# Kernel optimization log

Hardware: AMD Instinct MI355X
Metric: run time of the kernel (lower is better)

Reference implementation:

```python
import jax, jax.numpy as jnp
import numpy as np

SCALE = 1.0

def setup_inputs() -> dict:
    key = jax.random.key(0)
    k1, k2 = jax.random.split(key)
    template = jax.random.normal(k1, (4, 8192, 3), dtype=jnp.float32)
    source = jax.random.normal(k2, (4, 8192, 3), dtype=jnp.float32)
    return {"template": template, "source": source}

def _chamfer(p0, p1):
    # p0: [B,N,3], p1: [B,M,3]
    # squared pairwise distances: [B,N,M]
    sq0 = jnp.sum(p0 * p0, axis=-1)  # [B,N]
    sq1 = jnp.sum(p1 * p1, axis=-1)  # [B,M]
    cross = jnp.einsum('bnd,bmd->bnm', p0, p1)
    d = sq0[:, :, None] + sq1[:, None, :] - 2.0 * cross  # [B,N,M]
    d = jnp.maximum(d, 0.0)
    cost_p0_p1 = jnp.min(d, axis=2)  # [B,N] min sq dist p0 -> p1
    cost_p1_p0 = jnp.min(d, axis=1)  # [B,M] min sq dist p1 -> p0
    c01 = jnp.mean(jnp.sqrt(cost_p0_p1), axis=-1)  # [B]
    c10 = jnp.mean(jnp.sqrt(cost_p1_p0), axis=-1)  # [B]
    return (c01 + c10) / 2.0  # [B]

def reference(template, source):
    p0 = template / SCALE
    p1 = source / SCALE
    per_batch = _chamfer(p0, p1)
    return jnp.mean(per_batch, axis=0)  # reduction='mean' -> scalar
```

## Files before the change

kernel.cpp:

```cpp
#include <hip/hip_runtime.h>
#include <math.h>

#define NPTS 8192
#define NB 4
#define BLK 256
#define Q 8
#define TILE 512

__global__ __launch_bounds__(BLK) void chamfer_partial(
    const float* __restrict__ tmpl, const float* __restrict__ src,
    float* __restrict__ partial, int seg_len, int nseg)
{
    __shared__ float4 lds[TILE];
    const int bd  = blockIdx.z;
    const int b   = bd >> 1;
    const int dir = bd & 1;
    const float* qp = (dir ? src : tmpl) + (size_t)b * NPTS * 3;
    const float* rp = (dir ? tmpl : src) + (size_t)b * NPTS * 3;
    const int tid   = threadIdx.x;
    const int qbase = blockIdx.x * (BLK * Q);

    float qx[Q], qy[Q], qz[Q], mn[Q];
#pragma unroll
    for (int k = 0; k < Q; k++) {
        const int qi = qbase + k * BLK + tid;
        qx[k] = qp[3 * qi + 0];
        qy[k] = qp[3 * qi + 1];
        qz[k] = qp[3 * qi + 2];
        mn[k] = 3.4e38f;
    }

    const int seg_start = blockIdx.y * seg_len;
    for (int ts = 0; ts < seg_len; ts += TILE) {
        __syncthreads();
        for (int i = tid; i < TILE; i += BLK) {
            const int ri = seg_start + ts + i;
            const float rx = rp[3 * ri + 0];
            const float ry = rp[3 * ri + 1];
            const float rz = rp[3 * ri + 2];
            lds[i] = make_float4(-2.f * rx, -2.f * ry, -2.f * rz,
                                 rx * rx + ry * ry + rz * rz);
        }
        __syncthreads();
#pragma unroll 4
        for (int j = 0; j < TILE; j++) {
            const float4 r = lds[j];
#pragma unroll
            for (int k = 0; k < Q; k++) {
                float t = fmaf(qx[k], r.x, r.w);
                t = fmaf(qy[k], r.y, t);
                t = fmaf(qz[k], r.z, t);
                mn[k] = fminf(mn[k], t);
            }
        }
    }

    const size_t base = ((size_t)bd * nseg + blockIdx.y) * NPTS;
#pragma unroll
    for (int k = 0; k < Q; k++)
        partial[base + qbase + k * BLK + tid] = mn[k];
}

__global__ __launch_bounds__(BLK) void chamfer_reduce(
    const float* __restrict__ tmpl, const float* __restrict__ src,
    const float* __restrict__ partial, float* __restrict__ out, int nseg)
{
    const int t  = blockIdx.x * BLK + threadIdx.x;
    const int bd = t >> 13;
    const int qi = t & (NPTS - 1);
    const int b  = bd >> 1;
    const int dir = bd & 1;
    const float* qp = (dir ? src : tmpl) + (size_t)b * NPTS * 3;
    const float qx = qp[3 * qi + 0];
    const float qy = qp[3 * qi + 1];
    const float qz = qp[3 * qi + 2];
    const float sq = qx * qx + qy * qy + qz * qz;

    float m = 3.4e38f;
    for (int s = 0; s < nseg; s++)
        m = fminf(m, partial[((size_t)bd * nseg + s) * NPTS + qi]);

    float v = sqrtf(fmaxf(sq + m, 0.f));

#pragma unroll
    for (int off = 32; off > 0; off >>= 1)
        v += __shfl_down(v, off, 64);

    __shared__ float wsum[BLK / 64];
    const int lane = threadIdx.x & 63;
    const int wid  = threadIdx.x >> 6;
    if (lane == 0) wsum[wid] = v;
    __syncthreads();
    if (threadIdx.x == 0) {
        float s = 0.f;
#pragma unroll
        for (int w = 0; w < BLK / 64; w++) s += wsum[w];
        atomicAdd(out, s * (1.0f / 65536.0f));
    }
}

extern "C" void kernel_launch(void* const* d_in, const int* in_sizes, int n_in,
                              void* d_out, int out_size, void* d_ws, size_t ws_size,
                              hipStream_t stream) {
    const float* tmpl = (const float*)d_in[0];
    const float* src  = (const float*)d_in[1];
    float* out      = (float*)d_out;
    float* partial  = (float*)d_ws;

    int nseg = 16;
    while (nseg > 1 && (size_t)8 * nseg * NPTS * sizeof(float) > ws_size)
        nseg >>= 1;
    const int seg_len = NPTS / nseg;

    hipMemsetAsync(d_out, 0, sizeof(float), stream);

    dim3 g1(NPTS / (BLK * Q), nseg, 2 * NB);
    chamfer_partial<<<g1, BLK, 0, stream>>>(tmpl, src, partial, seg_len, nseg);

    chamfer_reduce<<<(2 * NB * NPTS) / BLK, BLK, 0, stream>>>(tmpl, src, partial, out, nseg);
}
```

Baseline: 105.3 us.

## Fuse partial-min and reduction kernels via last-block-done atomic ticket

Merges the two kernels into one launch. Each block writes its partial minima, then takes an atomic ticket per batch-direction, and the last block for that slice reduces all segments and sums the square roots. A second counter lets the final block write the output, which removes a kernel launch and the memset of the output. In exchange, the final reduction per slice runs serially in a single block, and the code relies on threadfence ordering. NSEG is now fixed and no longer adapts to the workspace size.

```diff
diff --git a/kernel.cpp b/kernel.cpp
--- a/kernel.cpp
+++ b/kernel.cpp
@@ -6,12 +6,24 @@
 #define BLK 256
 #define Q 8
 #define TILE 512
+#define NSEG 16
+#define QCHUNKS (NPTS / (BLK * Q))
+#define BLOCKS_PER_BD (NSEG * QCHUNKS)
+#define CTRL_FLOATS 64
 
-__global__ __launch_bounds__(BLK) void chamfer_partial(
+__global__ __launch_bounds__(BLK) void chamfer_fused(
     const float* __restrict__ tmpl, const float* __restrict__ src,
-    float* __restrict__ partial, int seg_len, int nseg)
+    float* __restrict__ ws, float* __restrict__ out)
 {
+    int*   cnt     = (int*)ws;
+    int*   cnt2    = (int*)ws + 8;
+    float* acc     = ws + 9;
+    float* partial = ws + CTRL_FLOATS;
+
     __shared__ float4 lds[TILE];
+    __shared__ float  wsum[BLK / 64];
+    __shared__ int    ticket;
+
     const int bd  = blockIdx.z;
     const int b   = bd >> 1;
     const int dir = bd & 1;
@@ -30,6 +42,7 @@
         mn[k] = 3.4e38f;
     }
 
+    const int seg_len   = NPTS / NSEG;
     const int seg_start = blockIdx.y * seg_len;
     for (int ts = 0; ts < seg_len; ts += TILE) {
         __syncthreads();
@@ -55,47 +68,51 @@
         }
     }
 
-    const size_t base = ((size_t)bd * nseg + blockIdx.y) * NPTS;
+    const size_t pbase = ((size_t)bd * NSEG + blockIdx.y) * NPTS;
 #pragma unroll
     for (int k = 0; k < Q; k++)
-        partial[base + qbase + k * BLK + tid] = mn[k];
-}
+        partial[pbase + qbase + k * BLK + tid] = mn[k];
 
-__global__ __launch_bounds__(BLK) void chamfer_reduce(
-    const float* __restrict__ tmpl, const float* __restrict__ src,
-    const float* __restrict__ partial, float* __restrict__ out, int nseg)
-{
-    const int t  = blockIdx.x * BLK + threadIdx.x;
-    const int bd = t >> 13;
-    const int qi = t & (NPTS - 1);
-    const int b  = bd >> 1;
-    const int dir = bd & 1;
-    const float* qp = (dir ? src : tmpl) + (size_t)b * NPTS * 3;
-    const float qx = qp[3 * qi + 0];
-    const float qy = qp[3 * qi + 1];
-    const float qz = qp[3 * qi + 2];
-    const float sq = qx * qx + qy * qy + qz * qz;
+    __threadfence();
+    __syncthreads();
+    if (tid == 0) ticket = atomicAdd(&cnt[bd], 1);
+    __syncthreads();
+    if (ticket != BLOCKS_PER_BD - 1) return;
+    __threadfence();
 
-    float m = 3.4e38f;
-    for (int s = 0; s < nseg; s++)
-        m = fminf(m, partial[((size_t)bd * nseg + s) * NPTS + qi]);
-
-    float v = sqrtf(fmaxf(sq + m, 0.f));
+    float sum = 0.f;
+    const size_t bdbase = (size_t)bd * NSEG * NPTS;
+#pragma unroll 2
+    for (int qb = 0; qb < NPTS / BLK; qb++) {
+        const int qi = qb * BLK + tid;
+        float m = partial[bdbase + qi];
+#pragma unroll
+        for (int s = 1; s < NSEG; s++)
+            m = fminf(m, partial[bdbase + (size_t)s * NPTS + qi]);
+        const float x = qp[3 * qi + 0];
+        const float y = qp[3 * qi + 1];
+        const float z = qp[3 * qi + 2];
+        sum += sqrtf(fmaxf(x * x + y * y + z * z + m, 0.f));
+    }
 
 #pragma unroll
     for (int off = 32; off > 0; off >>= 1)
-        v += __shfl_down(v, off, 64);
-
-    __shared__ float wsum[BLK / 64];
-    const int lane = threadIdx.x & 63;
-    const int wid  = threadIdx.x >> 6;
-    if (lane == 0) wsum[wid] = v;
+        sum += __shfl_down(sum, off, 64);
+    const int lane = tid & 63, wid = tid >> 6;
+    if (lane == 0) wsum[wid] = sum;
     __syncthreads();
-    if (threadIdx.x == 0) {
+    if (tid == 0) {
         float s = 0.f;
 #pragma unroll
         for (int w = 0; w < BLK / 64; w++) s += wsum[w];
-        atomicAdd(out, s * (1.0f / 65536.0f));
+        atomicAdd(acc, s);
+        __threadfence();
+        const int o2 = atomicAdd(cnt2, 1);
+        if (o2 == 2 * NB - 1) {
+            __threadfence();
+            const float tot = atomicAdd(acc, 0.0f);
+            *out = tot * (1.0f / 65536.0f);
+        }
     }
 }
 
@@ -104,18 +121,11 @@
                               hipStream_t stream) {
     const float* tmpl = (const float*)d_in[0];
     const float* src  = (const float*)d_in[1];
-    float* out      = (float*)d_out;
-    float* partial  = (float*)d_ws;
+    float* out = (float*)d_out;
+    float* ws  = (float*)d_ws;
 
-    int nseg = 16;
-    while (nseg > 1 && (size_t)8 * nseg * NPTS * sizeof(float) > ws_size)
-        nseg >>= 1;
-    const int seg_len = NPTS / nseg;
+    hipMemsetAsync(d_ws, 0, 64, stream);
 
-    hipMemsetAsync(d_out, 0, sizeof(float), stream);
-
-    dim3 g1(NPTS / (BLK * Q), nseg, 2 * NB);
-    chamfer_partial<<<g1, BLK, 0, stream>>>(tmpl, src, partial, seg_len, nseg);
-
-    chamfer_reduce<<<(2 * NB * NPTS) / BLK, BLK, 0, stream>>>(tmpl, src, partial, out, nseg);
+    dim3 grid(QCHUNKS, NSEG, 2 * NB);
+    chamfer_fused<<<grid, BLK, 0, stream>>>(tmpl, src, ws, out);
 }
```

Result: slower. 159.2 us (+51.2%).
